# Kernel tuning notes

Hardware: AMD Instinct MI355X
Metric: run time of the kernel (lower is better)

Reference implementation:

```python
import jax, jax.numpy as jnp
import numpy as np

N_FQK, N_FV, N_REL, N_VAL, N_KNOW = 512, 256, 128, 64, 256
TOPK_QK, TOPK_V, TOPK_REL, TOPK_VAL = 64, 32, 16, 3
FQK_END = N_FQK
FV_END = N_FQK + N_FV
REL_END = FV_END + N_REL
VAL_END = REL_END + N_VAL
TOTAL = VAL_END + N_KNOW


def setup_inputs() -> dict:
    key = jax.random.key(0)
    k1, k2, k3, k4, k5 = jax.random.split(key, 5)
    B, S, D, DS = 8, 4096, 1024, 64
    x = jax.random.normal(k1, (B, S, D), dtype=jnp.float32)
    importance = jax.random.uniform(k2, (B, S), dtype=jnp.float32)
    proj_w = jax.random.normal(k3, (DS, D), dtype=jnp.float32) * (1.0 / np.sqrt(D))
    proj_b = jax.random.normal(k4, (DS,), dtype=jnp.float32) * 0.01
    neuron_emb = jax.random.normal(k5, (TOTAL, DS), dtype=jnp.float32) * 0.02
    return {"x": x, "importance": importance, "proj_w": proj_w,
            "proj_b": proj_b, "neuron_emb": neuron_emb}


def _topk_sparsify(w, k):
    # keep top-k values per row, zero elsewhere
    vals, idx = jax.lax.top_k(w, k)
    B = w.shape[0]
    sparse = jnp.zeros_like(w).at[jnp.arange(B)[:, None], idx].set(vals)
    return sparse, idx


def reference(x, importance, proj_w, proj_b, neuron_emb):
    # shared projection + normalized neuron embeddings (eval: dropout off,
    # no excitability bonus)
    h = jnp.einsum('bsd,kd->bsk', x, proj_w) + proj_b          # [B,S,d_space]
    emb_n = neuron_emb / jnp.linalg.norm(neuron_emb, axis=-1, keepdims=True)
    all_logits = jnp.einsum('bsk,nk->bsn', h, emb_n)            # [B,S,TOTAL]

    def agg(logits):
        pref = jax.nn.softmax(logits, axis=-1)                  # [B,S,n]
        return jnp.einsum('bs,bsn->bn', importance, pref)

    w_qk = agg(all_logits[..., :FQK_END])
    _, idx_qk = jax.lax.top_k(w_qk, TOPK_QK)
    idx_qk = jnp.sort(idx_qk, axis=-1)

    w_v = agg(all_logits[..., FQK_END:FV_END])
    _, idx_v = jax.lax.top_k(w_v, TOPK_V)
    idx_v = jnp.sort(idx_v, axis=-1)

    rel_logits = all_logits[..., FV_END:REL_END]
    # relational_Q and relational_K use the same logits slice (eval mode)
    rel_dense_Q = agg(rel_logits)
    rel_dense_K = agg(rel_logits)
    rel_Q, _ = _topk_sparsify(rel_dense_Q, TOPK_REL)
    rel_K, _ = _topk_sparsify(rel_dense_K, TOPK_REL)

    val_dense = agg(all_logits[..., REL_END:VAL_END])
    val_w, _ = _topk_sparsify(val_dense, TOPK_VAL)

    return idx_qk, idx_v, rel_Q, rel_K, val_w
```

## Files before the change

kernel.cpp:

```cpp
#include <hip/hip_runtime.h>


typedef short short8 __attribute__((ext_vector_type(8)));
typedef float f32x4 __attribute__((ext_vector_type(4)));
typedef unsigned int uint4v __attribute__((ext_vector_type(4)));

__device__ __forceinline__ unsigned short f32_to_bf16(float f) {
  unsigned u = __float_as_uint(f);
  u += 0x7FFF + ((u >> 16) & 1);
  return (unsigned short)(u >> 16);
}
__device__ __forceinline__ float bf16_to_f32(unsigned short h) {
  return __uint_as_float(((unsigned)h) << 16);
}

__device__ __forceinline__ unsigned cvt_pk_bf16(float a, float b) {
  unsigned r;
  asm("v_cvt_pk_bf16_f32 %0, %1, %2" : "=v"(r) : "v"(a), "v"(b));
  return r;
}

__device__ __forceinline__ void split8v(const f32x4& v0, const f32x4& v1,
                                        short8& hi, short8& lo) {
  unsigned hp[4], lp[4];
#pragma unroll
  for (int j = 0; j < 4; ++j) {
    float a = (j < 2) ? v0[2 * j] : v1[2 * j - 4];
    float b = (j < 2) ? v0[2 * j + 1] : v1[2 * j - 3];
    unsigned p = cvt_pk_bf16(a, b);
    float ra = a - __uint_as_float(p << 16);
    float rb = b - __uint_as_float(p & 0xFFFF0000u);
    hp[j] = p;
    lp[j] = cvt_pk_bf16(ra, rb);
  }
  hi = __builtin_bit_cast(short8, (uint4v){hp[0], hp[1], hp[2], hp[3]});
  lo = __builtin_bit_cast(short8, (uint4v){lp[0], lp[1], lp[2], lp[3]});
}

#define MFMA(a, b, c) __builtin_amdgcn_mfma_f32_16x16x32_bf16(a, b, c, 0, 0, 0)

typedef const __attribute__((address_space(1))) unsigned int guint;
typedef __attribute__((address_space(3))) unsigned int luint;
__device__ __forceinline__ void stage16(const float* g, float* l) {
  __builtin_amdgcn_global_load_lds((guint*)g, (luint*)l, 16, 0, 0);
}
__device__ __forceinline__ void bar() {
  asm volatile("" ::: "memory");
  __builtin_amdgcn_s_barrier();
  asm volatile("" ::: "memory");
}

__global__ __launch_bounds__(256) void k_prep(const float* __restrict__ pw,
                                              const float* __restrict__ emb,
                                              unsigned short* __restrict__ whi,
                                              unsigned short* __restrict__ wlo,
                                              unsigned short* __restrict__ ehi,
                                              unsigned short* __restrict__ elo,
                                              float* __restrict__ wg) {
  int tid = blockIdx.x * 256 + threadIdx.x;
  if (tid < 7680) wg[tid] = 0.f;
  for (int i = tid; i < 65536; i += gridDim.x * 256) {
    float v = pw[i];
    unsigned short h = f32_to_bf16(v);
    whi[i] = h;
    wlo[i] = f32_to_bf16(v - bf16_to_f32(h));
  }
  int wid = tid >> 6, lane = tid & 63;
  int nw = gridDim.x * 4;
  for (int n = wid; n < 960; n += nw) {
    float v = emb[n * 64 + lane];
    float s = v * v;
#pragma unroll
    for (int off = 1; off < 64; off <<= 1) s += __shfl_xor(s, off);
    float vn = v / sqrtf(s);
    unsigned short h = f32_to_bf16(vn);
    ehi[n * 64 + lane] = h;
    elo[n * 64 + lane] = f32_to_bf16(vn - bf16_to_f32(h));
  }
}

__global__ __launch_bounds__(256, 4) void k_main(
    const float* __restrict__ x, const unsigned short* __restrict__ whi,
    const unsigned short* __restrict__ wlo, const float* __restrict__ pb,
    const unsigned short* __restrict__ ehi, const unsigned short* __restrict__ elo,
    const float* __restrict__ imp, float* __restrict__ wg) {
  __shared__ __align__(16) float xt[3][32][32];
  __shared__ __align__(16) unsigned short hxh[32][64];
  __shared__ __align__(16) unsigned short hxl[32][64];
  __shared__ float zpart[4][32][4];
  __shared__ float coefL[32][4];

  const int tid = threadIdx.x, w = tid >> 6, lane = tid & 63;
  const int q = lane >> 4, c = lane & 15;
  const int row0 = blockIdx.x * 32;
  const int nt0 = w;

  const int srow = tid >> 3;
  const int scol = ((tid & 7) ^ (srow & 7)) * 4;
  const float* sbase = x + (size_t)(row0 + srow) * 1024 + scol;
  auto STAGEX = [&](int slot, int ks) {
    stage16(sbase + ks * 32, &xt[slot][0][0] + (w << 8));
  };

  const unsigned short* bwh = whi + (size_t)(nt0 * 16 + c) * 1024 + q * 8;
  const unsigned short* bwl = wlo + (size_t)(nt0 * 16 + c) * 1024 + q * 8;

  f32x4 acc0 = {0.f, 0.f, 0.f, 0.f}, acc1 = {0.f, 0.f, 0.f, 0.f};

  const unsigned sw = (unsigned)((c & 7) << 4);
  const unsigned off1 = ((unsigned)(q * 32)) ^ sw;
  const unsigned off2 = ((unsigned)(q * 32 + 16)) ^ sw;
  const char* xby = (const char*)&xt[0][0][0] + (size_t)c * 128;

  auto projstep = [&](int slot, short8 B_hi, short8 B_lo) {
    const char* bp = xby + slot * 4096;
    f32x4 a0 = *(const f32x4*)(bp + off1);
    f32x4 a1 = *(const f32x4*)(bp + off2);
    f32x4 a2 = *(const f32x4*)(bp + 2048 + off1);
    f32x4 a3 = *(const f32x4*)(bp + 2048 + off2);
    short8 ah, al;
    split8v(a0, a1, ah, al);
    acc0 = MFMA(ah, B_hi, acc0);
    acc0 = MFMA(ah, B_lo, acc0);
    acc0 = MFMA(al, B_hi, acc0);
    split8v(a2, a3, ah, al);
    acc1 = MFMA(ah, B_hi, acc1);
    acc1 = MFMA(ah, B_lo, acc1);
    acc1 = MFMA(al, B_hi, acc1);
  };

  STAGEX(0, 0);
  STAGEX(1, 1);
  short8 bh = *(const short8*)bwh;
  short8 bl = *(const short8*)bwl;
  short8 bh_n, bl_n;
  int slot = 0;
  for (int ks = 0; ks < 30; ++ks) {
    int wslot = slot + 2; if (wslot >= 3) wslot -= 3;
    STAGEX(wslot, ks + 2);
    bh_n = *(const short8*)(bwh + (ks + 1) * 32);
    bl_n = *(const short8*)(bwl + (ks + 1) * 32);
    asm volatile("s_waitcnt vmcnt(6)" ::: "memory");
    bar();
    projstep(slot, bh, bl);
    bar();
    bh = bh_n; bl = bl_n;
    ++slot; if (slot == 3) slot = 0;
  }
  bh_n = *(const short8*)(bwh + 31 * 32);
  bl_n = *(const short8*)(bwl + 31 * 32);
  asm volatile("s_waitcnt vmcnt(5)" ::: "memory");
  bar();
  projstep(slot, bh, bl);
  bar();
  ++slot; if (slot == 3) slot = 0;
  asm volatile("s_waitcnt vmcnt(2)" ::: "memory");
  bar();
  projstep(slot, bh_n, bl_n);

  float bias = pb[nt0 * 16 + c];
#pragma unroll
  for (int mt = 0; mt < 2; ++mt) {
    f32x4 a = mt ? acc1 : acc0;
#pragma unroll
    for (int r = 0; r < 4; ++r) {
      float val = a[r] + bias;
      int row = mt * 16 + q * 4 + r;
      unsigned colb = (unsigned)((nt0 * 16 + c) * 2);
      unsigned o = (unsigned)(row * 128) + (colb ^ ((unsigned)(row & 7) << 4));
      unsigned short h = f32_to_bf16(val);
      *(unsigned short*)((char*)&hxh[0][0] + o) = h;
      *(unsigned short*)((char*)&hxl[0][0] + o) = f32_to_bf16(val - bf16_to_f32(h));
    }
  }
  __syncthreads();

  short8 Ahi[2][2], Alo[2][2];
#pragma unroll
  for (int mt = 0; mt < 2; ++mt) {
    int row = mt * 16 + c;
    unsigned rs = (unsigned)((row & 7) << 4);
#pragma unroll
    for (int k2 = 0; k2 < 2; ++k2) {
      unsigned o = (unsigned)(row * 128) + (((unsigned)(k2 * 64 + q * 16)) ^ rs);
      Ahi[mt][k2] = *(const short8*)((const char*)&hxh[0][0] + o);
      Alo[mt][k2] = *(const short8*)((const char*)&hxl[0][0] + o);
    }
  }

  const size_t ebq = (size_t)c * 64 + q * 8;
  auto ebase = [&](int i) { return (size_t)(w + 4 * i) * 1024 + ebq; };

  f32x4 zacc0 = {0.f, 0.f, 0.f, 0.f}, zacc1 = {0.f, 0.f, 0.f, 0.f};
  auto zflush = [&](int seg) {
#pragma unroll
    for (int mt = 0; mt < 2; ++mt)
#pragma unroll
      for (int r = 0; r < 4; ++r) {
        float v = mt ? zacc1[r] : zacc0[r];
        v += __shfl_xor(v, 1); v += __shfl_xor(v, 2);
        v += __shfl_xor(v, 4); v += __shfl_xor(v, 8);
        if (c == 0) zpart[w][mt * 16 + q * 4 + r][seg] = v;
      }
    zacc0 = (f32x4){0.f, 0.f, 0.f, 0.f};
    zacc1 = (f32x4){0.f, 0.f, 0.f, 0.f};
  };

  short8 e0h, e1h, e0l, e1l, n0h, n1h, n0l, n1l;
  {
    size_t eb = ebase(0);
    e0h = *(const short8*)(ehi + eb); e1h = *(const short8*)(ehi + eb + 32);
    e0l = *(const short8*)(elo + eb); e1l = *(const short8*)(elo + eb + 32);
  }
  int cur_seg = 0;
  for (int i = 0; i < 15; ++i) {
    int nt = w + 4 * i;
    int s = (nt < 32) ? 0 : (nt < 48) ? 1 : (nt < 56) ? 2 : 3;
    if (s != cur_seg) { zflush(cur_seg); cur_seg = s; }
    if (i < 14) {
      size_t eb = ebase(i + 1);
      n0h = *(const short8*)(ehi + eb); n1h = *(const short8*)(ehi + eb + 32);
      n0l = *(const short8*)(elo + eb); n1l = *(const short8*)(elo + eb + 32);
    }
#pragma unroll
    for (int mt = 0; mt < 2; ++mt) {
      f32x4 l = {0.f, 0.f, 0.f, 0.f};
      l = MFMA(Ahi[mt][0], e0h, l); l = MFMA(Ahi[mt][1], e1h, l);
      l = MFMA(Ahi[mt][0], e0l, l); l = MFMA(Ahi[mt][1], e1l, l);
      l = MFMA(Alo[mt][0], e0h, l); l = MFMA(Alo[mt][1], e1h, l);
#pragma unroll
      for (int r = 0; r < 4; ++r) {
        if (mt == 0) zacc0[r] += __expf(l[r]); else zacc1[r] += __expf(l[r]);
      }
    }
    e0h = n0h; e1h = n1h; e0l = n0l; e1l = n1l;
  }
  zflush(cur_seg);
  __syncthreads();
  if (tid < 128) {
    int row = tid & 31, sg = tid >> 5;
    float Z = zpart[0][row][sg] + zpart[1][row][sg] + zpart[2][row][sg] + zpart[3][row][sg];
    coefL[row][sg] = imp[row0 + row] / Z;
  }
  __syncthreads();

  const int bIdx = row0 >> 12;
  f32x4 cf0, cf1;
  int cs2 = -1;
  {
    size_t eb = ebase(0);
    e0h = *(const short8*)(ehi + eb); e1h = *(const short8*)(ehi + eb + 32);
    e0l = *(const short8*)(elo + eb); e1l = *(const short8*)(elo + eb + 32);
  }
  for (int i = 0; i < 15; ++i) {
    int nt = w + 4 * i;
    int s = (nt < 32) ? 0 : (nt < 48) ? 1 : (nt < 56) ? 2 : 3;
    if (s != cs2) {
#pragma unroll
      for (int r = 0; r < 4; ++r) {
        cf0[r] = coefL[q * 4 + r][s];
        cf1[r] = coefL[16 + q * 4 + r][s];
      }
      cs2 = s;
    }
    if (i < 14) {
      size_t eb = ebase(i + 1);
      n0h = *(const short8*)(ehi + eb); n1h = *(const short8*)(ehi + eb + 32);
      n0l = *(const short8*)(elo + eb); n1l = *(const short8*)(elo + eb + 32);
    }
    float wsum = 0.f;
#pragma unroll
    for (int mt = 0; mt < 2; ++mt) {
      f32x4 l = {0.f, 0.f, 0.f, 0.f};
      l = MFMA(Ahi[mt][0], e0h, l); l = MFMA(Ahi[mt][1], e1h, l);
      l = MFMA(Ahi[mt][0], e0l, l); l = MFMA(Ahi[mt][1], e1l, l);
      l = MFMA(Alo[mt][0], e0h, l); l = MFMA(Alo[mt][1], e1h, l);
#pragma unroll
      for (int r = 0; r < 4; ++r)
        wsum = fmaf(__expf(l[r]), mt ? cf1[r] : cf0[r], wsum);
    }
    wsum += __shfl_xor(wsum, 16);
    wsum += __shfl_xor(wsum, 32);
    if (lane < 16) atomicAdd(&wg[bIdx * 960 + nt * 16 + c], wsum);
    e0h = n0h; e1h = n1h; e0l = n0l; e1l = n1l;
  }
}

__global__ __launch_bounds__(256) void k_topk(const float* __restrict__ wg,
                                              float* __restrict__ out) {
  __shared__ float vals[512];
  __shared__ int flags[512];
  int blk = blockIdx.x;
  int b = blk >> 2, t = blk & 3;
  int tid = threadIdx.x;
  const int Ns[4] = {512, 256, 128, 64};
  const int Ks[4] = {64, 32, 16, 3};
  const int Off[4] = {0, 512, 768, 896};
  int N = Ns[t], K = Ks[t], off = Off[t];
  for (int n = tid; n < N; n += 256) vals[n] = wg[b * 960 + off + n];
  __syncthreads();
  for (int n = tid; n < N; n += 256) {
    float v = vals[n];
    int rank = 0;
    for (int m = 0; m < N; ++m) {
      float u = vals[m];
      rank += (u > v || (u == v && m < n)) ? 1 : 0;
    }
    flags[n] = (rank < K) ? 1 : 0;
  }
  __syncthreads();
  if (t <= 1) {
    if (tid < 64) {
      int base = 0;
      for (int ch = 0; ch < N; ch += 64) {
        int n = ch + tid;
        int f = flags[n];
        unsigned long long mask = __ballot(f);
        if (f) {
          int pos = base + __popcll(mask & ((1ull << tid) - 1ull));
          if (t == 0) out[b * 64 + pos] = (float)n;
          else out[512 + b * 32 + pos] = (float)n;
        }
        base += __popcll(mask);
      }
    }
  } else if (t == 2) {
    for (int n = tid; n < 128; n += 256) {
      float v = flags[n] ? vals[n] : 0.f;
      out[768 + b * 128 + n] = v;
      out[1792 + b * 128 + n] = v;
    }
  } else {
    for (int n = tid; n < 64; n += 256) {
      float v = flags[n] ? vals[n] : 0.f;
      out[2816 + b * 64 + n] = v;
    }
  }
}

extern "C" void kernel_launch(void* const* d_in, const int* in_sizes, int n_in,
                              void* d_out, int out_size, void* d_ws, size_t ws_size,
                              hipStream_t stream) {
  const float* x   = (const float*)d_in[0];
  const float* imp = (const float*)d_in[1];
  const float* pw  = (const float*)d_in[2];
  const float* pb  = (const float*)d_in[3];
  const float* emb = (const float*)d_in[4];
  float* out = (float*)d_out;

  char* ws = (char*)d_ws;
  unsigned short* whi = (unsigned short*)(ws);
  unsigned short* wlo = (unsigned short*)(ws + 131072);
  unsigned short* ehi = (unsigned short*)(ws + 262144);
  unsigned short* elo = (unsigned short*)(ws + 385024);
  float*          wg  = (float*)(ws + 507904);

  hipLaunchKernelGGL(k_prep, dim3(64), dim3(256), 0, stream, pw, emb, whi, wlo, ehi, elo, wg);
  hipLaunchKernelGGL(k_main, dim3(1024), dim3(256), 0, stream, x, whi, wlo, pb, ehi, elo, imp, wg);
  hipLaunchKernelGGL(k_topk, dim3(32), dim3(256), 0, stream, wg, out);
}
```

Measured before the change: 301.2 us.

## Deepen x staging ring to five slots and prefetch embeddings three ahead

The projection loop moves from a 3-slot LDS ring with one-step-ahead weight loads to a 5-slot ring with four tiles in flight. Weight fragments are fetched in groups of four into double-buffered register arrays, and the two barriers per step become one. Both logit passes now rotate three embedding register buffers, so each load is issued two tiles ahead. This aims to hide global-memory latency, at the cost of more shared memory and more registers, which could reduce occupancy.

```diff
diff --git a/kernel.cpp b/kernel.cpp
--- a/kernel.cpp
+++ b/kernel.cpp
@@ -84,7 +84,7 @@
     const unsigned short* __restrict__ wlo, const float* __restrict__ pb,
     const unsigned short* __restrict__ ehi, const unsigned short* __restrict__ elo,
     const float* __restrict__ imp, float* __restrict__ wg) {
-  __shared__ __align__(16) float xt[3][32][32];
+  __shared__ __align__(16) float xt[5][32][32];
   __shared__ __align__(16) unsigned short hxh[32][64];
   __shared__ __align__(16) unsigned short hxl[32][64];
   __shared__ float zpart[4][32][4];
@@ -129,34 +129,47 @@
     acc1 = MFMA(al, B_hi, acc1);
   };
 
-  STAGEX(0, 0);
-  STAGEX(1, 1);
-  short8 bh = *(const short8*)bwh;
-  short8 bl = *(const short8*)bwl;
-  short8 bh_n, bl_n;
-  int slot = 0;
-  for (int ks = 0; ks < 30; ++ks) {
-    int wslot = slot + 2; if (wslot >= 3) wslot -= 3;
-    STAGEX(wslot, ks + 2);
-    bh_n = *(const short8*)(bwh + (ks + 1) * 32);
-    bl_n = *(const short8*)(bwl + (ks + 1) * 32);
-    asm volatile("s_waitcnt vmcnt(6)" ::: "memory");
-    bar();
-    projstep(slot, bh, bl);
-    bar();
-    bh = bh_n; bl = bl_n;
-    ++slot; if (slot == 3) slot = 0;
-  }
-  bh_n = *(const short8*)(bwh + 31 * 32);
-  bl_n = *(const short8*)(bwl + 31 * 32);
-  asm volatile("s_waitcnt vmcnt(5)" ::: "memory");
-  bar();
-  projstep(slot, bh, bl);
-  bar();
-  ++slot; if (slot == 3) slot = 0;
-  asm volatile("s_waitcnt vmcnt(2)" ::: "memory");
-  bar();
-  projstep(slot, bh_n, bl_n);
+  short8 BhA[4], BlA[4], BhB[4], BlB[4];
+#pragma unroll
+  for (int kk = 0; kk < 4; ++kk) {
+    BhA[kk] = *(const short8*)(bwh + kk * 32);
+    BlA[kk] = *(const short8*)(bwl + kk * 32);
+  }
+  STAGEX(0, 0); STAGEX(1, 1); STAGEX(2, 2); STAGEX(3, 3);
+  int rs = 0, wsl = 4;
+
+  auto group = [&](int g, short8 (&ch)[4], short8 (&cl)[4],
+                   short8 (&nh)[4], short8 (&nl)[4]) {
+#pragma unroll
+    for (int kk = 0; kk < 4; ++kk) {
+      nh[kk] = *(const short8*)(bwh + ((g + 1) * 4 + kk) * 32);
+      nl[kk] = *(const short8*)(bwl + ((g + 1) * 4 + kk) * 32);
+    }
+#pragma unroll
+    for (int p = 0; p < 4; ++p) {
+      asm volatile("s_waitcnt vmcnt(11)" ::: "memory");
+      bar();
+      STAGEX(wsl, 4 * g + p + 4);
+      projstep(rs, ch[p], cl[p]);
+      ++rs; if (rs == 5) rs = 0;
+      ++wsl; if (wsl == 5) wsl = 0;
+    }
+  };
+  group(0, BhA, BlA, BhB, BlB);
+  group(1, BhB, BlB, BhA, BlA);
+  group(2, BhA, BlA, BhB, BlB);
+  group(3, BhB, BlB, BhA, BlA);
+  group(4, BhA, BlA, BhB, BlB);
+  group(5, BhB, BlB, BhA, BlA);
+  group(6, BhA, BlA, BhB, BlB);
+  asm volatile("s_waitcnt vmcnt(3)" ::: "memory"); bar();
+  projstep(rs, BhB[0], BlB[0]); ++rs; if (rs == 5) rs = 0;
+  asm volatile("s_waitcnt vmcnt(2)" ::: "memory"); bar();
+  projstep(rs, BhB[1], BlB[1]); ++rs; if (rs == 5) rs = 0;
+  asm volatile("s_waitcnt vmcnt(1)" ::: "memory"); bar();
+  projstep(rs, BhB[2], BlB[2]); ++rs; if (rs == 5) rs = 0;
+  asm volatile("s_waitcnt vmcnt(0)" ::: "memory"); bar();
+  projstep(rs, BhB[3], BlB[3]);
 
   float bias = pb[nt0 * 16 + c];
 #pragma unroll
@@ -179,17 +192,24 @@
 #pragma unroll
   for (int mt = 0; mt < 2; ++mt) {
     int row = mt * 16 + c;
-    unsigned rs = (unsigned)((row & 7) << 4);
+    unsigned rsw = (unsigned)((row & 7) << 4);
 #pragma unroll
     for (int k2 = 0; k2 < 2; ++k2) {
-      unsigned o = (unsigned)(row * 128) + (((unsigned)(k2 * 64 + q * 16)) ^ rs);
+      unsigned o = (unsigned)(row * 128) + (((unsigned)(k2 * 64 + q * 16)) ^ rsw);
       Ahi[mt][k2] = *(const short8*)((const char*)&hxh[0][0] + o);
       Alo[mt][k2] = *(const short8*)((const char*)&hxl[0][0] + o);
     }
   }
 
   const size_t ebq = (size_t)c * 64 + q * 8;
-  auto ebase = [&](int i) { return (size_t)(w + 4 * i) * 1024 + ebq; };
+  short8 eA[4], eB[4], eC[4];
+  auto LOADE = [&](short8 (&d)[4], int i) {
+    size_t eb = (size_t)(w + 4 * i) * 1024 + ebq;
+    d[0] = *(const short8*)(ehi + eb);
+    d[1] = *(const short8*)(ehi + eb + 32);
+    d[2] = *(const short8*)(elo + eb);
+    d[3] = *(const short8*)(elo + eb + 32);
+  };
 
   f32x4 zacc0 = {0.f, 0.f, 0.f, 0.f}, zacc1 = {0.f, 0.f, 0.f, 0.f};
   auto zflush = [&](int seg) {
@@ -206,34 +226,28 @@
     zacc1 = (f32x4){0.f, 0.f, 0.f, 0.f};
   };
 
-  short8 e0h, e1h, e0l, e1l, n0h, n1h, n0l, n1l;
-  {
-    size_t eb = ebase(0);
-    e0h = *(const short8*)(ehi + eb); e1h = *(const short8*)(ehi + eb + 32);
-    e0l = *(const short8*)(elo + eb); e1l = *(const short8*)(elo + eb + 32);
-  }
   int cur_seg = 0;
-  for (int i = 0; i < 15; ++i) {
+  auto step1 = [&](int i, short8 (&e)[4]) {
     int nt = w + 4 * i;
     int s = (nt < 32) ? 0 : (nt < 48) ? 1 : (nt < 56) ? 2 : 3;
     if (s != cur_seg) { zflush(cur_seg); cur_seg = s; }
-    if (i < 14) {
-      size_t eb = ebase(i + 1);
-      n0h = *(const short8*)(ehi + eb); n1h = *(const short8*)(ehi + eb + 32);
-      n0l = *(const short8*)(elo + eb); n1l = *(const short8*)(elo + eb + 32);
-    }
 #pragma unroll
     for (int mt = 0; mt < 2; ++mt) {
       f32x4 l = {0.f, 0.f, 0.f, 0.f};
-      l = MFMA(Ahi[mt][0], e0h, l); l = MFMA(Ahi[mt][1], e1h, l);
-      l = MFMA(Ahi[mt][0], e0l, l); l = MFMA(Ahi[mt][1], e1l, l);
-      l = MFMA(Alo[mt][0], e0h, l); l = MFMA(Alo[mt][1], e1h, l);
+      l = MFMA(Ahi[mt][0], e[0], l); l = MFMA(Ahi[mt][1], e[1], l);
+      l = MFMA(Ahi[mt][0], e[2], l); l = MFMA(Ahi[mt][1], e[3], l);
+      l = MFMA(Alo[mt][0], e[0], l); l = MFMA(Alo[mt][1], e[1], l);
 #pragma unroll
       for (int r = 0; r < 4; ++r) {
         if (mt == 0) zacc0[r] += __expf(l[r]); else zacc1[r] += __expf(l[r]);
       }
     }
-    e0h = n0h; e1h = n1h; e0l = n0l; e1l = n1l;
+  };
+  LOADE(eA, 0); LOADE(eB, 1);
+  for (int j = 0; j < 5; ++j) {
+    LOADE(eC, 3 * j + 2);            step1(3 * j, eA);
+    if (j < 4) LOADE(eA, 3 * j + 3); step1(3 * j + 1, eB);
+    if (j < 4) LOADE(eB, 3 * j + 4); step1(3 * j + 2, eC);
   }
   zflush(cur_seg);
   __syncthreads();
@@ -247,12 +261,7 @@
   const int bIdx = row0 >> 12;
   f32x4 cf0, cf1;
   int cs2 = -1;
-  {
-    size_t eb = ebase(0);
-    e0h = *(const short8*)(ehi + eb); e1h = *(const short8*)(ehi + eb + 32);
-    e0l = *(const short8*)(elo + eb); e1l = *(const short8*)(elo + eb + 32);
-  }
-  for (int i = 0; i < 15; ++i) {
+  auto step2 = [&](int i, short8 (&e)[4]) {
     int nt = w + 4 * i;
     int s = (nt < 32) ? 0 : (nt < 48) ? 1 : (nt < 56) ? 2 : 3;
     if (s != cs2) {
@@ -263,18 +272,13 @@
       }
       cs2 = s;
     }
-    if (i < 14) {
-      size_t eb = ebase(i + 1);
-      n0h = *(const short8*)(ehi + eb); n1h = *(const short8*)(ehi + eb + 32);
-      n0l = *(const short8*)(elo + eb); n1l = *(const short8*)(elo + eb + 32);
-    }
     float wsum = 0.f;
 #pragma unroll
     for (int mt = 0; mt < 2; ++mt) {
       f32x4 l = {0.f, 0.f, 0.f, 0.f};
-      l = MFMA(Ahi[mt][0], e0h, l); l = MFMA(Ahi[mt][1], e1h, l);
-      l = MFMA(Ahi[mt][0], e0l, l); l = MFMA(Ahi[mt][1], e1l, l);
-      l = MFMA(Alo[mt][0], e0h, l); l = MFMA(Alo[mt][1], e1h, l);
+      l = MFMA(Ahi[mt][0], e[0], l); l = MFMA(Ahi[mt][1], e[1], l);
+      l = MFMA(Ahi[mt][0], e[2], l); l = MFMA(Ahi[mt][1], e[3], l);
+      l = MFMA(Alo[mt][0], e[0], l); l = MFMA(Alo[mt][1], e[1], l);
 #pragma unroll
       for (int r = 0; r < 4; ++r)
         wsum = fmaf(__expf(l[r]), mt ? cf1[r] : cf0[r], wsum);
@@ -282,7 +286,12 @@
     wsum += __shfl_xor(wsum, 16);
     wsum += __shfl_xor(wsum, 32);
     if (lane < 16) atomicAdd(&wg[bIdx * 960 + nt * 16 + c], wsum);
-    e0h = n0h; e1h = n1h; e0l = n0l; e1l = n1l;
+  };
+  LOADE(eA, 0); LOADE(eB, 1);
+  for (int j = 0; j < 5; ++j) {
+    LOADE(eC, 3 * j + 2);            step2(3 * j, eA);
+    if (j < 4) LOADE(eA, 3 * j + 3); step2(3 * j + 1, eB);
+    if (j < 4) LOADE(eB, 3 * j + 4); step2(3 * j + 2, eC);
   }
 }
 
```

After: 302.4 us. About the same (+0.4%).
